# Kernel tuning notes

Hardware: AMD Instinct MI355X
Metric: run time of the kernel (lower is better)

The kernel has to match this reference:

```python
import jax, jax.numpy as jnp
import numpy as np

D = 768       # input_dim / model width
H = 3072      # expert hidden width (init arg 'output_dim')
E = 8         # num_experts
K = 2         # top_k
NOISE_STD = 0.1
B, S = 2, 1024


def setup_inputs() -> dict:
    key = jax.random.key(0)
    ks = jax.random.split(key, 16)
    sd = lambda fan_in: 1.0 / np.sqrt(fan_in)
    return {
        "x": jax.random.normal(ks[0], (B, S, D), dtype=jnp.float32),
        "noise": jax.random.normal(ks[1], (B, S, E), dtype=jnp.float32),
        # router
        "Wr": jax.random.normal(ks[2], (D, E), dtype=jnp.float32) * sd(D),
        "br": jnp.zeros((E,), dtype=jnp.float32),
        # stacked expert FFNs: d -> h -> d
        "W1": jax.random.normal(ks[3], (E, D, H), dtype=jnp.float32) * sd(D),
        "b1": jnp.zeros((E, H), dtype=jnp.float32),
        "W2": jax.random.normal(ks[4], (E, H, D), dtype=jnp.float32) * sd(H),
        "b2": jnp.zeros((E, D), dtype=jnp.float32),
        # shared expert
        "Ws1": jax.random.normal(ks[5], (D, H), dtype=jnp.float32) * sd(D),
        "bs1": jnp.zeros((H,), dtype=jnp.float32),
        "Ws2": jax.random.normal(ks[6], (H, D), dtype=jnp.float32) * sd(H),
        "bs2": jnp.zeros((D,), dtype=jnp.float32),
        # mixing scalars (alpha trainable, beta frozen in torch)
        "alpha": jnp.float32(0.3),
        "beta": jnp.float32(0.7),
    }


def reference(x, noise, Wr, br, W1, b1, W2, b2, Ws1, bs1, Ws2, bs2, alpha, beta):
    b, s, d = x.shape
    xt = x.reshape(-1, d)                       # [T, D]
    nt = noise.reshape(-1, E)                   # [T, E]
    T = xt.shape[0]

    # router: noisy logits -> top-k -> softmax over selected experts only
    logits = xt @ Wr + br + NOISE_STD * nt      # [T, E]
    top_vals, top_idx = jax.lax.top_k(logits, K)  # [T, K]
    top_w = jax.nn.softmax(top_vals, axis=-1)     # softmax over -inf-masked logits == softmax over top-k
    gates = jnp.zeros((T, E), dtype=x.dtype).at[jnp.arange(T)[:, None], top_idx].set(top_w)  # [T, E], 0 elsewhere

    # experts (dense over E; non-selected contributions are zeroed by gates)
    h = jax.nn.leaky_relu(jnp.einsum('td,edh->teh', xt, W1) + b1, negative_slope=0.01)  # [T, E, H]
    y = jnp.einsum('teh,ehd->ted', h, W2) + b2                                          # [T, E, D]
    moe_out = jnp.einsum('ted,te->td', y, gates)                                        # [T, D]

    # shared expert
    sh = jax.nn.leaky_relu(xt @ Ws1 + bs1, negative_slope=0.01)
    shared_out = sh @ Ws2 + bs2                                                         # [T, D]

    w = jax.nn.softmax(jnp.stack([alpha, beta]))
    out = shared_out * w[0] + moe_out * w[1]
    return out.reshape(b, s, d)
```

## Files before the change

kernel.cpp:

```cpp
#include <hip/hip_runtime.h>
#include <hip/hip_bf16.h>
#include <cstdio>
#include <cstdint>

#define TNUM 2048
#define DDIM 768
#define HDIM 3072
#define ENUM 8

#define WAITVM(N) asm volatile("s_waitcnt vmcnt(" #N ")" ::: "memory")
#define WAITLGKM() asm volatile("s_waitcnt lgkmcnt(0)" ::: "memory")
#define MEMFENCE() asm volatile("" ::: "memory")

typedef __attribute__((ext_vector_type(8))) __bf16 bf16x8;
typedef __attribute__((ext_vector_type(4))) float f32x4;

__device__ __forceinline__ unsigned short f2bf(float f) {
    __bf16 h = (__bf16)f;
    unsigned short u;
    __builtin_memcpy(&u, &h, 2);
    return u;
}

__device__ __forceinline__ void async_cp16(const unsigned short* g, unsigned short* l) {
    __builtin_amdgcn_global_load_lds((const __attribute__((address_space(1))) void*)g,
                                     (__attribute__((address_space(3))) void*)l,
                                     16, 0, 0);
}

__device__ __forceinline__ void transpose_tile(const float* __restrict__ in,
                                               unsigned short* __restrict__ out,
                                               int R, int C, int c0, int r0,
                                               unsigned int* tileT32) {
    int tid = threadIdx.x;
    int l15 = tid & 15;
    int g = tid >> 4;
    int par = (g >> 1) & 1;
    int hf = g & 1;
    int cb = hf * 64 + l15 * 4;
    const float* src = in + (size_t)(r0 + (g >> 1)) * C + c0 + cb;
    float4 v[16];
    #pragma unroll
    for (int p = 0; p < 16; p++)
        v[p] = *(const float4*)(src + (size_t)p * 8 * C);
    #pragma unroll
    for (int p = 0; p < 16; p++) {
        int unit = p * 16 + g;
        unsigned int m01 = (unsigned int)f2bf(v[p].x) | ((unsigned int)f2bf(v[p].y) << 16);
        unsigned int m23 = (unsigned int)f2bf(v[p].z) | ((unsigned int)f2bf(v[p].w) << 16);
        unsigned int o01 = __shfl_xor(m01, 32);
        unsigned int o23 = __shfl_xor(m23, 32);
        unsigned int wA = par ? ((o23 & 0xffffu) | (m23 << 16))
                              : ((m01 & 0xffffu) | (o01 << 16));
        unsigned int wB = par ? ((o23 >> 16) | (m23 & 0xffff0000u))
                              : ((m01 >> 16) | (o01 & 0xffff0000u));
        int ca = cb + par * 2;
        int rp = unit >> 2;
        int cq = ca >> 2;
        int woff = 4 * (((rp >> 2) + 3 * cq) & 15) + (((rp & 3) + cq) & 3);
        tileT32[ca * 68 + woff] = wA;
        tileT32[(ca + 1) * 68 + woff] = wB;
    }
    __syncthreads();
    uint4 Wv[8];
    #pragma unroll
    for (int p = 0; p < 8; p++) {
        int cc = p * 16 + g;
        int cqp = cc >> 2;
        Wv[p] = *(const uint4*)&tileT32[cc * 68 + 4 * ((l15 + 3 * cqp) & 15)];
    }
    #pragma unroll
    for (int p = 0; p < 8; p++) {
        int cc = p * 16 + g;
        int cqp = cc >> 2;
        unsigned int a0 = Wv[p].x, a1 = Wv[p].y, a2 = Wv[p].z, a3 = Wv[p].w;
        int rsel = cqp & 3;
        if (rsel & 1) { unsigned int t = a0; a0 = a1; a1 = a2; a2 = a3; a3 = t; }
        if (rsel & 2) { unsigned int t0 = a0, t1 = a1; a0 = a2; a1 = a3; a2 = t0; a3 = t1; }
        uint4 ov; ov.x = a0; ov.y = a1; ov.z = a2; ov.w = a3;
        *(uint4*)(out + (size_t)(c0 + cc) * R + r0 + l15 * 8) = ov;
    }
}

__global__ __launch_bounds__(256, 4)
void pre_kernel(const float* __restrict__ x, const float* __restrict__ noise,
                const float* __restrict__ Wr, const float* __restrict__ br,
                const float* __restrict__ W2, const float* __restrict__ Ws2,
                unsigned short* __restrict__ W2t, unsigned short* __restrict__ Ws2t,
                unsigned short* __restrict__ xb,
                int* __restrict__ counts, int* __restrict__ list,
                int* __restrict__ inv, float* __restrict__ tokp) {
    __shared__ __align__(16) unsigned int tileT32[128 * 68];
    int b = blockIdx.x;
    if (b < 1296) {
        int m = b / 144, t = b % 144;
        const float* in     = (m < 8) ? (W2 + (size_t)m * HDIM * DDIM) : Ws2;
        unsigned short* out = (m < 8) ? (W2t + (size_t)m * DDIM * HDIM) : Ws2t;
        transpose_tile(in, out, HDIM, DDIM, (t % 6) * 128, (t / 6) * 128, tileT32);
        return;
    }
    if (b < 2064) {
        int i = ((b - 1296) * 256 + threadIdx.x) * 8;
        float4 a = *(const float4*)(x + i);
        float4 bb = *(const float4*)(x + i + 4);
        ushort4 lo = make_ushort4(f2bf(a.x), f2bf(a.y), f2bf(a.z), f2bf(a.w));
        ushort4 hi = make_ushort4(f2bf(bb.x), f2bf(bb.y), f2bf(bb.z), f2bf(bb.w));
        *(ushort4*)(xb + i) = lo;
        *(ushort4*)(xb + i + 4) = hi;
        return;
    }
    int lane = threadIdx.x & 63;
    int t = (b - 2064) * 4 + (threadIdx.x >> 6);
    float acc[8];
    #pragma unroll
    for (int e = 0; e < 8; e++) acc[e] = 0.f;
    #pragma unroll
    for (int i = 0; i < 12; i++) {
        int d = i * 64 + lane;
        float xv = x[t * DDIM + d];
        float4 w0 = *(const float4*)(Wr + d * 8);
        float4 w1 = *(const float4*)(Wr + d * 8 + 4);
        acc[0] += xv * w0.x; acc[1] += xv * w0.y; acc[2] += xv * w0.z; acc[3] += xv * w0.w;
        acc[4] += xv * w1.x; acc[5] += xv * w1.y; acc[6] += xv * w1.z; acc[7] += xv * w1.w;
    }
    #pragma unroll
    for (int e = 0; e < 8; e++) {
        #pragma unroll
        for (int off2 = 32; off2 >= 1; off2 >>= 1)
            acc[e] += __shfl_xor(acc[e], off2, 64);
    }
    if (lane == 0) {
        float lg[8];
        #pragma unroll
        for (int e = 0; e < 8; e++) lg[e] = acc[e] + br[e] + 0.1f * noise[t * 8 + e];
        int e0 = 0;
        #pragma unroll
        for (int e = 1; e < 8; e++) if (lg[e] > lg[e0]) e0 = e;
        int e1 = -1;
        #pragma unroll
        for (int e = 0; e < 8; e++) if (e != e0 && (e1 < 0 || lg[e] > lg[e1])) e1 = e;
        float m = fmaxf(lg[e0], lg[e1]);
        float p0 = expf(lg[e0] - m), p1 = expf(lg[e1] - m);
        float inv_s = 1.f / (p0 + p1);
        int s0 = atomicAdd(&counts[e0], 1);
        list[e0 * TNUM + s0] = t;
        int s1 = atomicAdd(&counts[e1], 1);
        list[e1 * TNUM + s1] = t;
        inv[t * 2 + 0] = (e0 << 16) | s0;
        inv[t * 2 + 1] = (e1 << 16) | s1;
        tokp[t * 2 + 0] = p0 * inv_s;
        tokp[t * 2 + 1] = p1 * inv_s;
    }
}

__global__ __launch_bounds__(256, 3)
void ffn1_kernel(const unsigned short* __restrict__ xb,
                 const float* __restrict__ W1,
                 const float* __restrict__ Ws1,
                 const float* __restrict__ b1, const float* __restrict__ bs1,
                 const int* __restrict__ counts, const int* __restrict__ list,
                 unsigned short* __restrict__ hbuf) {
    __shared__ __align__(16) unsigned short As[2][512 * 8];
    __shared__ __align__(16) unsigned int Bs32[2048];

    int j = blockIdx.z * 8 + blockIdx.x;
    int y = blockIdx.y;
    int mt0 = y / 6, ntl = y % 6;

    int offv[8];
    { int s = 0;
      #pragma unroll
      for (int e = 0; e < 8; e++) { offv[e] = s; s += counts[e]; } }

    int cnt, hbase, n0, mbase, ntiles;
    const float* Bf;
    const float* bias;
    const int* lst = nullptr;
    if (j < 32) {
        int e = j >> 2, nq = j & 3;
        cnt = counts[e];
        ntiles = (cnt + 127) >> 7;
        mbase = 0;
        hbase = offv[e];
        n0 = nq * 768 + ntl * 128;
        Bf = W1 + (size_t)e * DDIM * HDIM;
        bias = b1 + e * HDIM;
        lst = list + e * TNUM;
    } else {
        int q = j - 32;
        int ms = q >> 2, nq = q & 3;
        mbase = ms * 1024;
        ntiles = 8;
        cnt = 1 << 30;
        hbase = 2 * TNUM;
        n0 = nq * 768 + ntl * 128;
        Bf = Ws1;
        bias = bs1;
    }
    if (mt0 >= ntiles) return;

    int tid = threadIdx.x;
    int w = tid >> 6, lane = tid & 63;
    int l15 = lane & 15, quad = lane >> 4;
    int wm = (w & 1) * 64, wn = (w >> 1) * 64;
    int rcA = (w & 1) * 4;
    int rcB = (w >> 1) * 4;
    const int KT = DDIM / 32;

    int l31 = tid & 31;
    int rp0 = tid >> 5;
    int nlh = l31 >> 2;
    int nll4 = (l31 & 3) * 4;
    int c4 = l31 * 4;

    int ldsoff[2], rowl[2];
    #pragma unroll
    for (int r = 0; r < 2; r++) {
        int rc = r * 4 + w;
        rowl[r] = rc * 16 + l15;
        ldsoff[r] = rc * 512;
    }

    for (int mt = mt0; mt < ntiles; mt += 4) {
        int m0 = mbase + mt * 128;
        const unsigned short* gA[2];
        #pragma unroll
        for (int r = 0; r < 2; r++) {
            int row;
            if (lst) row = lst[min(m0 + rowl[r], cnt - 1)];
            else     row = m0 + rowl[r];
            gA[r] = xb + (size_t)row * DDIM + quad * 8;
        }

        f32x4 zero = {0.f, 0.f, 0.f, 0.f};
        f32x4 acc[4][4];
        #pragma unroll
        for (int i = 0; i < 4; i++)
            #pragma unroll
            for (int jj = 0; jj < 4; jj++) acc[i][jj] = zero;

        #pragma unroll
        for (int r = 0; r < 2; r++) async_cp16(gA[r], &As[0][ldsoff[r]]);
        float4 Ba[2], Bb[2];
        #pragma unroll
        for (int p = 0; p < 2; p++) {
            const float* bp = Bf + (size_t)(2 * (p * 8 + rp0)) * HDIM + n0 + c4;
            Ba[p] = *(const float4*)bp;
            Bb[p] = *(const float4*)(bp + HDIM);
        }

        #pragma unroll 1
        for (int kt = 0; kt < KT; kt++) {
            int cur = kt & 1;
            WAITVM(0);
            #pragma unroll
            for (int p = 0; p < 2; p++) {
                int kp = p * 8 + rp0;
                int gb = ((nlh * 64 + (kp >> 2) * 16 + nll4) << 2) + ((kp + nlh) & 3);
                float4 a = Ba[p], b = Bb[p];
                Bs32[gb + 0]  = (unsigned int)f2bf(a.x) | ((unsigned int)f2bf(b.x) << 16);
                Bs32[gb + 4]  = (unsigned int)f2bf(a.y) | ((unsigned int)f2bf(b.y) << 16);
                Bs32[gb + 8]  = (unsigned int)f2bf(a.z) | ((unsigned int)f2bf(b.z) << 16);
                Bs32[gb + 12] = (unsigned int)f2bf(a.w) | ((unsigned int)f2bf(b.w) << 16);
            }
            if (kt + 1 < KT) {
                int ko = (kt + 1) * 32;
                #pragma unroll
                for (int r = 0; r < 2; r++)
                    async_cp16(gA[r] + ko, &As[cur ^ 1][ldsoff[r]]);
                #pragma unroll
                for (int p = 0; p < 2; p++) {
                    const float* bp = Bf + (size_t)(ko + 2 * (p * 8 + rp0)) * HDIM + n0 + c4;
                    Ba[p] = *(const float4*)bp;
                    Bb[p] = *(const float4*)(bp + HDIM);
                }
            }
            WAITLGKM();
            __builtin_amdgcn_s_barrier();
            MEMFENCE();
            bf16x8 af[4], bv[4];
            #pragma unroll
            for (int i = 0; i < 4; i++)
                af[i] = *(const bf16x8*)&As[cur][((rcA + i) * 64 + quad * 16 + l15) * 8];
            #pragma unroll
            for (int jj = 0; jj < 4; jj++) {
                uint4 Wv = *(const uint4*)&Bs32[((rcB + jj) * 64 + quad * 16 + l15) << 2];
                unsigned int s0 = Wv.x, s1 = Wv.y, s2 = Wv.z, s3 = Wv.w;
                unsigned int t0, t1, t2, t3;
                if (jj == 0)      { t0 = s0; t1 = s1; t2 = s2; t3 = s3; }
                else if (jj == 1) { t0 = s1; t1 = s2; t2 = s3; t3 = s0; }
                else if (jj == 2) { t0 = s2; t1 = s3; t2 = s0; t3 = s1; }
                else              { t0 = s3; t1 = s0; t2 = s1; t3 = s2; }
                uint4 L; L.x = t0; L.y = t1; L.z = t2; L.w = t3;
                __builtin_memcpy(&bv[jj], &L, 16);
            }
            #pragma unroll
            for (int i = 0; i < 4; i++)
                #pragma unroll
                for (int jj = 0; jj < 4; jj++)
                    acc[i][jj] = __builtin_amdgcn_mfma_f32_16x16x32_bf16(af[i], bv[jj], acc[i][jj], 0, 0, 0);
            MEMFENCE();
            __builtin_amdgcn_s_barrier();
            MEMFENCE();
        }

        #pragma unroll
        for (int i = 0; i < 4; i++) {
            int rbase = m0 + wm + i * 16 + quad * 4;
            #pragma unroll
            for (int jj = 0; jj < 4; jj++) {
                int gc = n0 + wn + jj * 16 + l15;
                float bvl = bias[gc];
                #pragma unroll
                for (int r = 0; r < 4; r++) {
                    int gr = rbase + r;
                    if (gr < cnt) {
                        float v = acc[i][jj][r] + bvl;
                        v = v > 0.f ? v : 0.01f * v;
                        hbuf[(size_t)(hbase + gr) * HDIM + gc] = f2bf(v);
                    }
                }
            }
        }
    }
}

__global__ __launch_bounds__(256, 4)
void ffn2_kernel(const unsigned short* __restrict__ hbuf,
                 const unsigned short* __restrict__ W2t,
                 const unsigned short* __restrict__ Ws2t,
                 const int* __restrict__ counts,
                 float* __restrict__ ybuf) {
    __shared__ __align__(16) unsigned short As[2][512 * 8];
    __shared__ __align__(16) unsigned short Bs[2][512 * 8];

    int j = blockIdx.z * 8 + blockIdx.x;
    int y = blockIdx.y;
    int mt0 = y / 6, ntl = y % 6;
    int n0 = ntl * 128;

    int offv[8];
    { int s = 0;
      #pragma unroll
      for (int e = 0; e < 8; e++) { offv[e] = s; s += counts[e]; } }

    int cnt, hbase, mbase, kh, ntiles;
    const unsigned short* Bmat;
    if (j < 16) {
        int e = j >> 1; kh = j & 1;
        cnt = counts[e];
        ntiles = (cnt + 127) >> 7;
        mbase = 0;
        hbase = offv[e];
        Bmat = W2t + (size_t)e * DDIM * HDIM;
    } else {
        int q = j - 16;
        int ms = q >> 1; kh = q & 1;
        mbase = ms * 512;
        ntiles = 4;
        cnt = 1 << 30;
        hbase = 2 * TNUM;
        Bmat = Ws2t;
    }
    if (mt0 >= ntiles) return;
    int kbase = kh * (HDIM / 2);

    int tid = threadIdx.x;
    int w = tid >> 6, lane = tid & 63;
    int l15 = lane & 15, quad = lane >> 4;
    int wm = (w & 1) * 64, wn = (w >> 1) * 64;
    int rcA = (w & 1) * 4;
    int rcB = (w >> 1) * 4;
    const int KT = (HDIM / 2) / 32;

    const unsigned short* gB[2];
    int ldsoff[2], rowl[2];
    #pragma unroll
    for (int r = 0; r < 2; r++) {
        int rc = r * 4 + w;
        rowl[r] = rc * 16 + l15;
        ldsoff[r] = rc * 512;
        gB[r] = Bmat + (size_t)(n0 + rowl[r]) * HDIM + kbase + quad * 8;
    }
    float* yb = ybuf + (size_t)kh * 6144 * DDIM;

    for (int mt = mt0; mt < ntiles; mt += 4) {
        int m0 = mbase + mt * 128;
        const unsigned short* gA[2];
        #pragma unroll
        for (int r = 0; r < 2; r++) {
            int row = (j < 16) ? min(m0 + rowl[r], cnt - 1) : (m0 + rowl[r]);
            gA[r] = hbuf + (size_t)(hbase + row) * HDIM + kbase + quad * 8;
        }

        f32x4 zero = {0.f, 0.f, 0.f, 0.f};
        f32x4 acc[4][4];
        #pragma unroll
        for (int i = 0; i < 4; i++)
            #pragma unroll
            for (int jj = 0; jj < 4; jj++) acc[i][jj] = zero;

        #pragma unroll
        for (int t = 0; t < 2; t++)
            #pragma unroll
            for (int r = 0; r < 2; r++) {
                async_cp16(gA[r] + t * 32, &As[t][ldsoff[r]]);
                async_cp16(gB[r] + t * 32, &Bs[t][ldsoff[r]]);
            }

        #pragma unroll 1
        for (int kt = 0; kt < KT; kt++) {
            if (kt == KT - 1) { WAITVM(0); } else { WAITVM(4); }
            __builtin_amdgcn_s_barrier();
            MEMFENCE();
            int cur = kt & 1;
            bf16x8 af[4], bv[4];
            #pragma unroll
            for (int i = 0; i < 4; i++)
                af[i] = *(const bf16x8*)&As[cur][((rcA + i) * 64 + quad * 16 + l15) * 8];
            #pragma unroll
            for (int jj = 0; jj < 4; jj++)
                bv[jj] = *(const bf16x8*)&Bs[cur][((rcB + jj) * 64 + quad * 16 + l15) * 8];
            #pragma unroll
            for (int i = 0; i < 4; i++)
                #pragma unroll
                for (int jj = 0; jj < 4; jj++)
                    acc[i][jj] = __builtin_amdgcn_mfma_f32_16x16x32_bf16(af[i], bv[jj], acc[i][jj], 0, 0, 0);
            MEMFENCE();
            __builtin_amdgcn_s_barrier();
            MEMFENCE();
            if (kt + 2 < KT) {
                int ko = (kt + 2) * 32;
                #pragma unroll
                for (int r = 0; r < 2; r++) {
                    async_cp16(gA[r] + ko, &As[cur][ldsoff[r]]);
                    async_cp16(gB[r] + ko, &Bs[cur][ldsoff[r]]);
                }
            }
        }

        #pragma unroll
        for (int i = 0; i < 4; i++) {
            int rbase = m0 + wm + i * 16 + quad * 4;
            #pragma unroll
            for (int r = 0; r < 4; r++) {
                int gr = rbase + r;
                if (gr >= cnt) continue;
                float* orow = yb + (size_t)(hbase + gr) * DDIM + n0 + wn;
                #pragma unroll
                for (int jj = 0; jj < 4; jj++)
                    orow[jj * 16 + l15] = acc[i][jj][r];
            }
        }
    }
}

__global__ void mix_kernel(const float* __restrict__ ybuf, const int* __restrict__ inv,
                           const float* __restrict__ tokp, const int* __restrict__ counts,
                           const float* __restrict__ b2, const float* __restrict__ bs2,
                           const float* __restrict__ alpha, const float* __restrict__ beta,
                           float* __restrict__ out) {
    int t = blockIdx.x;
    int c = threadIdx.x * 4;
    int offv[8];
    { int s = 0;
      #pragma unroll
      for (int e = 0; e < 8; e++) { offv[e] = s; s += counts[e]; } }
    float a = alpha[0], bsc = beta[0];
    float m = fmaxf(a, bsc);
    float ea = expf(a - m), eb = expf(bsc - m);
    float is = 1.f / (ea + eb);
    float ws = ea * is, wmx = eb * is;

    int i0 = inv[t * 2 + 0], i1 = inv[t * 2 + 1];
    int e0 = i0 >> 16, sl0 = i0 & 0xFFFF;
    int e1 = i1 >> 16, sl1 = i1 & 0xFFFF;
    float p0 = tokp[t * 2 + 0], p1 = tokp[t * 2 + 1];
    size_t rA = (size_t)(offv[e0] + sl0) * DDIM + c;
    size_t rB = (size_t)(offv[e1] + sl1) * DDIM + c;
    size_t rS = (size_t)(2 * TNUM + t) * DDIM + c;
    const float* y0 = ybuf;
    const float* y1 = ybuf + (size_t)6144 * DDIM;
    float4 vA0 = *(const float4*)(y0 + rA);
    float4 vA1 = *(const float4*)(y1 + rA);
    float4 vB0 = *(const float4*)(y0 + rB);
    float4 vB1 = *(const float4*)(y1 + rB);
    float4 vS0 = *(const float4*)(y0 + rS);
    float4 vS1 = *(const float4*)(y1 + rS);
    float4 bA = *(const float4*)(b2 + e0 * DDIM + c);
    float4 bB = *(const float4*)(b2 + e1 * DDIM + c);
    float4 bS = *(const float4*)(bs2 + c);
    float4 o;
    o.x = ws * (vS0.x + vS1.x + bS.x) + wmx * (p0 * (vA0.x + vA1.x + bA.x) + p1 * (vB0.x + vB1.x + bB.x));
    o.y = ws * (vS0.y + vS1.y + bS.y) + wmx * (p0 * (vA0.y + vA1.y + bA.y) + p1 * (vB0.y + vB1.y + bB.y));
    o.z = ws * (vS0.z + vS1.z + bS.z) + wmx * (p0 * (vA0.z + vA1.z + bA.z) + p1 * (vB0.z + vB1.z + bB.z));
    o.w = ws * (vS0.w + vS1.w + bS.w) + wmx * (p0 * (vA0.w + vA1.w + bA.w) + p1 * (vB0.w + vB1.w + bB.w));
    *(float4*)(out + (size_t)t * DDIM + c) = o;
}

extern "C" void kernel_launch(void* const* d_in, const int* in_sizes, int n_in,
                              void* d_out, int out_size, void* d_ws, size_t ws_size,
                              hipStream_t stream) {
    const float* x     = (const float*)d_in[0];
    const float* noise = (const float*)d_in[1];
    const float* Wr    = (const float*)d_in[2];
    const float* br    = (const float*)d_in[3];
    const float* W1    = (const float*)d_in[4];
    const float* b1    = (const float*)d_in[5];
    const float* W2    = (const float*)d_in[6];
    const float* b2    = (const float*)d_in[7];
    const float* Ws1   = (const float*)d_in[8];
    const float* bs1   = (const float*)d_in[9];
    const float* Ws2   = (const float*)d_in[10];
    const float* bs2   = (const float*)d_in[11];
    const float* alpha = (const float*)d_in[12];
    const float* beta  = (const float*)d_in[13];

    char* ws = (char*)d_ws;
    size_t off = 0;
    auto alloc = [&](size_t bytes) -> char* {
        char* p = ws + off;
        off = (off + bytes + 255) & ~(size_t)255;
        return p;
    };
    int*   counts = (int*)  alloc(ENUM * 4);
    int*   list   = (int*)  alloc((size_t)ENUM * TNUM * 4);
    int*   inv    = (int*)  alloc((size_t)TNUM * 2 * 4);
    float* tokp   = (float*)alloc((size_t)TNUM * 2 * 4);
    unsigned short* xb   = (unsigned short*)alloc((size_t)TNUM * DDIM * 2);
    float* ybuf          = (float*)alloc((size_t)2 * 6144 * DDIM * 4);
    unsigned short* W2t  = (unsigned short*)alloc((size_t)ENUM * DDIM * HDIM * 2);
    unsigned short* Ws2t = (unsigned short*)alloc((size_t)DDIM * HDIM * 2);
    unsigned short* hbuf = (unsigned short*)alloc((size_t)(3 * TNUM) * HDIM * 2);
    if (off > ws_size) {
        fprintf(stderr, "kernel_launch: workspace too small (need %zu, have %zu)\n", off, ws_size);
        return;
    }

    hipMemsetAsync(counts, 0, ENUM * 4, stream);

    pre_kernel<<<dim3(2576), dim3(256), 0, stream>>>(x, noise, Wr, br, W2, Ws2,
                                                     W2t, Ws2t, xb, counts, list, inv, tokp);
    ffn1_kernel<<<dim3(8, 24, 5), dim3(256), 0, stream>>>(xb, W1, Ws1, b1, bs1, counts, list, hbuf);
    ffn2_kernel<<<dim3(8, 24, 3), dim3(256), 0, stream>>>(hbuf, W2t, Ws2t, counts, ybuf);
    mix_kernel<<<dim3(TNUM), dim3(192), 0, stream>>>(ybuf, inv, tokp, counts, b2, bs2,
                                                     alpha, beta, (float*)d_out);
}
```

Before: 435.0 us.

## Deepen ffn1 K-loop prefetch to three stages with triple-buffered A tiles

The ffn1 GEMM main loop moves from a two-stage pipeline that drained all memory ops every step (vmcnt(0)) to a three-stage pipeline. A tiles are triple-buffered in LDS and two register sets hold B weight prefetches, issued two k-steps ahead. The loop is unrolled by six via a macro, and a partial vmcnt(6) wait leaves the next stage's loads in flight. This is meant to hide global memory latency better. It costs extra VGPRs and LDS, which under launch_bounds(256,3) could force spills or lower occupancy, and it assumes KT is a multiple of six.

```diff
diff --git a/kernel.cpp b/kernel.cpp
--- a/kernel.cpp
+++ b/kernel.cpp
@@ -153,6 +153,61 @@
     }
 }
 
+#define FFN1_STEP(KIDX, BA, BB, BUF)                                              \
+    {                                                                             \
+        const int kt_ = (KIDX);                                                   \
+        if (kt_ == KT - 1) { WAITVM(0); } else { WAITVM(6); }                     \
+        _Pragma("unroll")                                                         \
+        for (int p = 0; p < 2; p++) {                                             \
+            int kp = p * 8 + rp0;                                                 \
+            int gb = ((nlh * 64 + (kp >> 2) * 16 + nll4) << 2) + ((kp + nlh) & 3);\
+            float4 pa = BA[p], pb = BB[p];                                        \
+            Bs32[gb + 0]  = (unsigned int)f2bf(pa.x) | ((unsigned int)f2bf(pb.x) << 16); \
+            Bs32[gb + 4]  = (unsigned int)f2bf(pa.y) | ((unsigned int)f2bf(pb.y) << 16); \
+            Bs32[gb + 8]  = (unsigned int)f2bf(pa.z) | ((unsigned int)f2bf(pb.z) << 16); \
+            Bs32[gb + 12] = (unsigned int)f2bf(pa.w) | ((unsigned int)f2bf(pb.w) << 16); \
+        }                                                                         \
+        if (kt_ + 2 < KT) {                                                       \
+            int ko = (kt_ + 2) * 32;                                              \
+            _Pragma("unroll")                                                     \
+            for (int r = 0; r < 2; r++)                                           \
+                async_cp16(gA[r] + ko, &As[((BUF) + 2) % 3][ldsoff[r]]);          \
+            _Pragma("unroll")                                                     \
+            for (int p = 0; p < 2; p++) {                                         \
+                const float* bp = Bf + (size_t)(ko + 2 * (p * 8 + rp0)) * HDIM + n0 + c4; \
+                BA[p] = *(const float4*)bp;                                       \
+                BB[p] = *(const float4*)(bp + HDIM);                              \
+            }                                                                     \
+        }                                                                         \
+        WAITLGKM();                                                               \
+        __builtin_amdgcn_s_barrier();                                             \
+        MEMFENCE();                                                               \
+        bf16x8 af[4], bv[4];                                                      \
+        _Pragma("unroll")                                                         \
+        for (int i = 0; i < 4; i++)                                               \
+            af[i] = *(const bf16x8*)&As[(BUF)][((rcA + i) * 64 + quad * 16 + l15) * 8]; \
+        _Pragma("unroll")                                                         \
+        for (int jj = 0; jj < 4; jj++) {                                          \
+            uint4 Wv = *(const uint4*)&Bs32[((rcB + jj) * 64 + quad * 16 + l15) << 2]; \
+            unsigned int s0 = Wv.x, s1 = Wv.y, s2 = Wv.z, s3 = Wv.w;              \
+            unsigned int t0, t1, t2, t3;                                          \
+            if (jj == 0)      { t0 = s0; t1 = s1; t2 = s2; t3 = s3; }             \
+            else if (jj == 1) { t0 = s1; t1 = s2; t2 = s3; t3 = s0; }             \
+            else if (jj == 2) { t0 = s2; t1 = s3; t2 = s0; t3 = s1; }             \
+            else              { t0 = s3; t1 = s0; t2 = s1; t3 = s2; }             \
+            uint4 L; L.x = t0; L.y = t1; L.z = t2; L.w = t3;                      \
+            __builtin_memcpy(&bv[jj], &L, 16);                                    \
+        }                                                                         \
+        _Pragma("unroll")                                                         \
+        for (int i = 0; i < 4; i++)                                               \
+            _Pragma("unroll")                                                     \
+            for (int jj = 0; jj < 4; jj++)                                        \
+                acc[i][jj] = __builtin_amdgcn_mfma_f32_16x16x32_bf16(af[i], bv[jj], acc[i][jj], 0, 0, 0); \
+        MEMFENCE();                                                               \
+        __builtin_amdgcn_s_barrier();                                             \
+        MEMFENCE();                                                               \
+    }
+
 __global__ __launch_bounds__(256, 3)
 void ffn1_kernel(const unsigned short* __restrict__ xb,
                  const float* __restrict__ W1,
@@ -160,7 +215,7 @@
                  const float* __restrict__ b1, const float* __restrict__ bs1,
                  const int* __restrict__ counts, const int* __restrict__ list,
                  unsigned short* __restrict__ hbuf) {
-    __shared__ __align__(16) unsigned short As[2][512 * 8];
+    __shared__ __align__(16) unsigned short As[3][512 * 8];
     __shared__ __align__(16) unsigned int Bs32[2048];
 
     int j = blockIdx.z * 8 + blockIdx.x;
@@ -239,69 +294,33 @@
             #pragma unroll
             for (int jj = 0; jj < 4; jj++) acc[i][jj] = zero;
 
+        float4 Ba0[2], Bb0[2], Ba1[2], Bb1[2];
         #pragma unroll
         for (int r = 0; r < 2; r++) async_cp16(gA[r], &As[0][ldsoff[r]]);
-        float4 Ba[2], Bb[2];
         #pragma unroll
         for (int p = 0; p < 2; p++) {
             const float* bp = Bf + (size_t)(2 * (p * 8 + rp0)) * HDIM + n0 + c4;
-            Ba[p] = *(const float4*)bp;
-            Bb[p] = *(const float4*)(bp + HDIM);
+            Ba0[p] = *(const float4*)bp;
+            Bb0[p] = *(const float4*)(bp + HDIM);
+        }
+        MEMFENCE();
+        #pragma unroll
+        for (int r = 0; r < 2; r++) async_cp16(gA[r] + 32, &As[1][ldsoff[r]]);
+        #pragma unroll
+        for (int p = 0; p < 2; p++) {
+            const float* bp = Bf + (size_t)(32 + 2 * (p * 8 + rp0)) * HDIM + n0 + c4;
+            Ba1[p] = *(const float4*)bp;
+            Bb1[p] = *(const float4*)(bp + HDIM);
         }
 
         #pragma unroll 1
-        for (int kt = 0; kt < KT; kt++) {
-            int cur = kt & 1;
-            WAITVM(0);
-            #pragma unroll
-            for (int p = 0; p < 2; p++) {
-                int kp = p * 8 + rp0;
-                int gb = ((nlh * 64 + (kp >> 2) * 16 + nll4) << 2) + ((kp + nlh) & 3);
-                float4 a = Ba[p], b = Bb[p];
-                Bs32[gb + 0]  = (unsigned int)f2bf(a.x) | ((unsigned int)f2bf(b.x) << 16);
-                Bs32[gb + 4]  = (unsigned int)f2bf(a.y) | ((unsigned int)f2bf(b.y) << 16);
-                Bs32[gb + 8]  = (unsigned int)f2bf(a.z) | ((unsigned int)f2bf(b.z) << 16);
-                Bs32[gb + 12] = (unsigned int)f2bf(a.w) | ((unsigned int)f2bf(b.w) << 16);
-            }
-            if (kt + 1 < KT) {
-                int ko = (kt + 1) * 32;
-                #pragma unroll
-                for (int r = 0; r < 2; r++)
-                    async_cp16(gA[r] + ko, &As[cur ^ 1][ldsoff[r]]);
-                #pragma unroll
-                for (int p = 0; p < 2; p++) {
-                    const float* bp = Bf + (size_t)(ko + 2 * (p * 8 + rp0)) * HDIM + n0 + c4;
-                    Ba[p] = *(const float4*)bp;
-                    Bb[p] = *(const float4*)(bp + HDIM);
-                }
-            }
-            WAITLGKM();
-            __builtin_amdgcn_s_barrier();
-            MEMFENCE();
-            bf16x8 af[4], bv[4];
-            #pragma unroll
-            for (int i = 0; i < 4; i++)
-                af[i] = *(const bf16x8*)&As[cur][((rcA + i) * 64 + quad * 16 + l15) * 8];
-            #pragma unroll
-            for (int jj = 0; jj < 4; jj++) {
-                uint4 Wv = *(const uint4*)&Bs32[((rcB + jj) * 64 + quad * 16 + l15) << 2];
-                unsigned int s0 = Wv.x, s1 = Wv.y, s2 = Wv.z, s3 = Wv.w;
-                unsigned int t0, t1, t2, t3;
-                if (jj == 0)      { t0 = s0; t1 = s1; t2 = s2; t3 = s3; }
-                else if (jj == 1) { t0 = s1; t1 = s2; t2 = s3; t3 = s0; }
-                else if (jj == 2) { t0 = s2; t1 = s3; t2 = s0; t3 = s1; }
-                else              { t0 = s3; t1 = s0; t2 = s1; t3 = s2; }
-                uint4 L; L.x = t0; L.y = t1; L.z = t2; L.w = t3;
-                __builtin_memcpy(&bv[jj], &L, 16);
-            }
-            #pragma unroll
-            for (int i = 0; i < 4; i++)
-                #pragma unroll
-                for (int jj = 0; jj < 4; jj++)
-                    acc[i][jj] = __builtin_amdgcn_mfma_f32_16x16x32_bf16(af[i], bv[jj], acc[i][jj], 0, 0, 0);
-            MEMFENCE();
-            __builtin_amdgcn_s_barrier();
-            MEMFENCE();
+        for (int kt6 = 0; kt6 < KT; kt6 += 6) {
+            FFN1_STEP(kt6 + 0, Ba0, Bb0, 0)
+            FFN1_STEP(kt6 + 1, Ba1, Bb1, 1)
+            FFN1_STEP(kt6 + 2, Ba0, Bb0, 2)
+            FFN1_STEP(kt6 + 3, Ba1, Bb1, 0)
+            FFN1_STEP(kt6 + 4, Ba0, Bb0, 1)
+            FFN1_STEP(kt6 + 5, Ba1, Bb1, 2)
         }
 
         #pragma unroll
```

Measured after the change: 451.8 us. +3.9%, slower.
